# Kernel optimization log

Measured on AMD Instinct MI355X. Metric: run time of the kernel, lower is better.

## Reference

```python
import jax, jax.numpy as jnp
import numpy as np

TEMPERATURE = 0.07
N, D, NUM_CLASSES = 8192, 1024, 128


def setup_inputs() -> dict:
    key = jax.random.key(0)
    k1, k2 = jax.random.split(key)
    embeddings = jax.random.normal(k1, (N, D), dtype=jnp.float32)
    labels = jax.random.randint(k2, (N,), 0, NUM_CLASSES, dtype=jnp.int64)
    return {"embeddings": embeddings, "labels": labels}


def reference(embeddings, labels):
    # L2-normalize rows (eps matches F.normalize default clamp of 1e-12 on the norm)
    norm = jnp.maximum(jnp.linalg.norm(embeddings, axis=-1, keepdims=True), 1e-12)
    emb = embeddings / norm
    # [N, N] similarity scaled by temperature
    sim = jnp.matmul(emb, emb.T) / TEMPERATURE
    # positive mask: same label, diagonal zeroed
    pos_mask = (labels[:, None] == labels[None, :]).astype(sim.dtype)
    pos_mask = pos_mask * (1.0 - jnp.eye(sim.shape[0], dtype=sim.dtype))
    exp_sim = jnp.exp(sim)
    sum_exp = exp_sim.sum(axis=1)              # [N]
    pos_sum = (exp_sim * pos_mask).sum(axis=1)  # [N]
    loss = -jnp.log(pos_sum / sum_exp)
    return loss.mean()
```

## Files before the change

### kernel.cpp

```cpp
#include <hip/hip_runtime.h>
#include <hip/hip_bf16.h>
#include <math.h>

#define N 8192
#define D 1024
#define TILE 128
#define BK 32
#define NTILES (N / TILE)
#define NBLOCKS (NTILES * (NTILES + 1) / 2)

typedef __bf16 bf16_t;
typedef bf16_t bf16x4 __attribute__((ext_vector_type(4)));
typedef bf16_t bf16x8 __attribute__((ext_vector_type(8)));
typedef float f32x4 __attribute__((ext_vector_type(4)));

__global__ __launch_bounds__(256) void norm_cast(const float* __restrict__ in,
                                                 bf16_t* __restrict__ out) {
    const int row = blockIdx.x;
    const int tid = threadIdx.x;
    const float4 v = ((const float4*)(in + (size_t)row * D))[tid];
    float ss = v.x * v.x + v.y * v.y + v.z * v.z + v.w * v.w;
    #pragma unroll
    for (int off = 32; off >= 1; off >>= 1) ss += __shfl_xor(ss, off, 64);
    __shared__ float red[4];
    const int wave = tid >> 6, lane = tid & 63;
    if (lane == 0) red[wave] = ss;
    __syncthreads();
    const float tot = red[0] + red[1] + red[2] + red[3];
    const float scale = 1.0f / fmaxf(sqrtf(tot), 1e-12f);
    bf16x4 o;
    o[0] = (bf16_t)(v.x * scale);
    o[1] = (bf16_t)(v.y * scale);
    o[2] = (bf16_t)(v.z * scale);
    o[3] = (bf16_t)(v.w * scale);
    ((bf16x4*)(out + (size_t)row * D))[tid] = o;
}

__global__ __launch_bounds__(256) void gemm_fused(const bf16_t* __restrict__ E,
                                                  const int* __restrict__ labels,
                                                  float* __restrict__ sumExp,
                                                  float* __restrict__ posSum) {
    __shared__ bf16_t As[TILE * BK];
    __shared__ bf16_t Bs[TILE * BK];
    __shared__ int labR[TILE], labC[TILE];

    const int b = blockIdx.x;
    int ti = (int)((sqrtf(8.0f * (float)b + 1.0f) - 1.0f) * 0.5f);
    while ((ti + 1) * (ti + 2) / 2 <= b) ++ti;
    while (ti * (ti + 1) / 2 > b) --ti;
    const int tj = b - ti * (ti + 1) / 2;
    const bool isDiag = (ti == tj);

    const int tid     = threadIdx.x;
    const int wave    = tid >> 6;
    const int lane    = tid & 63;
    const int q       = lane >> 4;
    const int lr      = lane & 15;
    const int waveRow = wave >> 1;
    const int waveCol = wave & 1;
    const int rowStart = ti * TILE;
    const int colStart = tj * TILE;

    if (tid < TILE) labR[tid] = labels[rowStart + tid];
    else            labC[tid - TILE] = labels[colStart + (tid - TILE)];

    f32x4 acc[4][4];
    #pragma unroll
    for (int i = 0; i < 4; ++i)
        #pragma unroll
        for (int j = 0; j < 4; ++j)
            acc[i][j] = {0.f, 0.f, 0.f, 0.f};

    const char* baseA = (const char*)(E + (size_t)rowStart * D);
    const char* baseB = (const char*)(E + (size_t)colStart * D);

    const int runit = q ^ ((lr >> 1) & 3);

    for (int kk = 0; kk < D; kk += BK) {
        #pragma unroll
        for (int p = 0; p < 2; ++p) {
            const int u  = p * 256 + tid;
            const int r  = u >> 2;
            const int uc = (u & 3) ^ ((r >> 1) & 3);
            const char* ga = baseA + (size_t)r * (D * 2) + kk * 2 + uc * 16;
            const char* gb = baseB + (size_t)r * (D * 2) + kk * 2 + uc * 16;
            char* la = (char*)As + (p * 256 + wave * 64) * 16;
            char* lb = (char*)Bs + (p * 256 + wave * 64) * 16;
            __builtin_amdgcn_global_load_lds(
                (const __attribute__((address_space(1))) void*)ga,
                (__attribute__((address_space(3))) void*)la, 16, 0, 0);
            __builtin_amdgcn_global_load_lds(
                (const __attribute__((address_space(1))) void*)gb,
                (__attribute__((address_space(3))) void*)lb, 16, 0, 0);
        }
        __syncthreads();

        bf16x8 af[4], bfr[4];
        #pragma unroll
        for (int ri = 0; ri < 4; ++ri)
            af[ri] = *(const bf16x8*)((const char*)As +
                     (waveRow * 64 + ri * 16 + lr) * 64 + runit * 16);
        #pragma unroll
        for (int ci = 0; ci < 4; ++ci)
            bfr[ci] = *(const bf16x8*)((const char*)Bs +
                      (waveCol * 64 + ci * 16 + lr) * 64 + runit * 16);
        #pragma unroll
        for (int ri = 0; ri < 4; ++ri)
            #pragma unroll
            for (int ci = 0; ci < 4; ++ci)
                acc[ri][ci] = __builtin_amdgcn_mfma_f32_16x16x32_bf16(
                    af[ri], bfr[ci], acc[ri][ci], 0, 0, 0);
        __syncthreads();
    }

    const float invT = 1.0f / 0.07f;
    float colAll[4] = {0.f, 0.f, 0.f, 0.f};
    float colPos[4] = {0.f, 0.f, 0.f, 0.f};
    #pragma unroll
    for (int ri = 0; ri < 4; ++ri) {
        #pragma unroll
        for (int e = 0; e < 4; ++e) {
            const int rloc = waveRow * 64 + ri * 16 + q * 4 + e;
            const int gi   = rowStart + rloc;
            const int li   = labR[rloc];
            float s_all = 0.f, s_pos = 0.f;
            #pragma unroll
            for (int ci = 0; ci < 4; ++ci) {
                const int cloc = waveCol * 64 + ci * 16 + lr;
                const int gj   = colStart + cloc;
                const float v  = __expf(acc[ri][ci][e] * invT);
                const bool same = (labC[cloc] == li);
                s_all += v;
                if (same && gi != gj) s_pos += v;
                if (!isDiag) {
                    colAll[ci] += v;
                    if (same) colPos[ci] += v;
                }
            }
            #pragma unroll
            for (int off = 1; off < 16; off <<= 1) {
                s_all += __shfl_xor(s_all, off, 64);
                s_pos += __shfl_xor(s_pos, off, 64);
            }
            if (lr == 0) {
                atomicAdd(&sumExp[gi], s_all);
                atomicAdd(&posSum[gi], s_pos);
            }
        }
    }
    if (!isDiag) {
        #pragma unroll
        for (int ci = 0; ci < 4; ++ci) {
            float a = colAll[ci], p = colPos[ci];
            a += __shfl_xor(a, 16, 64);  a += __shfl_xor(a, 32, 64);
            p += __shfl_xor(p, 16, 64);  p += __shfl_xor(p, 32, 64);
            if (q == 0) {
                const int gj = colStart + waveCol * 64 + ci * 16 + lr;
                atomicAdd(&sumExp[gj], a);
                atomicAdd(&posSum[gj], p);
            }
        }
    }
}

__global__ __launch_bounds__(1024) void finalize(const float* __restrict__ sumExp,
                                                 const float* __restrict__ posSum,
                                                 float* __restrict__ out) {
    const int tid = threadIdx.x;
    float s = 0.f;
    #pragma unroll
    for (int i = tid; i < N; i += 1024)
        s += __logf(sumExp[i] / posSum[i]);
    #pragma unroll
    for (int off = 32; off >= 1; off >>= 1) s += __shfl_xor(s, off, 64);
    __shared__ float red[16];
    if ((tid & 63) == 0) red[tid >> 6] = s;
    __syncthreads();
    if (tid == 0) {
        float t = 0.f;
        #pragma unroll
        for (int i = 0; i < 16; ++i) t += red[i];
        out[0] = t / (float)N;
    }
}

extern "C" void kernel_launch(void* const* d_in, const int* in_sizes, int n_in,
                              void* d_out, int out_size, void* d_ws, size_t ws_size,
                              hipStream_t stream) {
    const float* emb    = (const float*)d_in[0];
    const int*   labels = (const int*)d_in[1];
    float* out = (float*)d_out;

    float*  sumExp = (float*)d_ws;
    float*  posSum = sumExp + N;
    bf16_t* EN     = (bf16_t*)((char*)d_ws + (size_t)2 * N * sizeof(float));

    hipMemsetAsync(d_ws, 0, (size_t)2 * N * sizeof(float), stream);

    norm_cast<<<N, 256, 0, stream>>>(emb, EN);

    gemm_fused<<<NBLOCKS, 256, 0, stream>>>(EN, labels, sumExp, posSum);

    finalize<<<1, 1024, 0, stream>>>(sumExp, posSum, out);
}
```

Measured before the change: 217.3 us.

## Load MFMA fragments directly from global memory, fold temperature into normalization, reorder tiles

Removes the LDS staging in the fused GEMM. Each wave now loads its bf16 MFMA fragments straight from global memory into registers with double buffering and no barriers in the K loop. The temperature and log2(e) factor are folded into the normalization scale (sqrt(log2e/T) per row), so the epilogue uses a raw exp2 instead of a multiply plus exp. Block-to-tile mapping is changed to group tiles in 8-wide column bands to improve L2 reuse, and a missing sync after the label loads is added. The cost is that rows are read redundantly from global/L2 by multiple waves with no LDS sharing, and pre-scaling before the bf16 cast changes rounding slightly.

```diff
diff --git a/kernel.cpp b/kernel.cpp
--- a/kernel.cpp
+++ b/kernel.cpp
@@ -5,7 +5,6 @@
 #define N 8192
 #define D 1024
 #define TILE 128
-#define BK 32
 #define NTILES (N / TILE)
 #define NBLOCKS (NTILES * (NTILES + 1) / 2)
 
@@ -13,6 +12,8 @@
 typedef bf16_t bf16x4 __attribute__((ext_vector_type(4)));
 typedef bf16_t bf16x8 __attribute__((ext_vector_type(8)));
 typedef float f32x4 __attribute__((ext_vector_type(4)));
+
+#define POST_SCALE 4.5398124f
 
 __global__ __launch_bounds__(256) void norm_cast(const float* __restrict__ in,
                                                  bf16_t* __restrict__ out) {
@@ -27,7 +28,7 @@
     if (lane == 0) red[wave] = ss;
     __syncthreads();
     const float tot = red[0] + red[1] + red[2] + red[3];
-    const float scale = 1.0f / fmaxf(sqrtf(tot), 1e-12f);
+    const float scale = POST_SCALE / fmaxf(sqrtf(tot), 1e-12f);
     bf16x4 o;
     o[0] = (bf16_t)(v.x * scale);
     o[1] = (bf16_t)(v.y * scale);
@@ -40,15 +41,24 @@
                                                   const int* __restrict__ labels,
                                                   float* __restrict__ sumExp,
                                                   float* __restrict__ posSum) {
-    __shared__ bf16_t As[TILE * BK];
-    __shared__ bf16_t Bs[TILE * BK];
     __shared__ int labR[TILE], labC[TILE];
 
     const int b = blockIdx.x;
-    int ti = (int)((sqrtf(8.0f * (float)b + 1.0f) - 1.0f) * 0.5f);
-    while ((ti + 1) * (ti + 2) / 2 <= b) ++ti;
-    while (ti * (ti + 1) / 2 > b) --ti;
-    const int tj = b - ti * (ti + 1) / 2;
+    int c = (int)((sqrtf(16.0f + 128.0f * (float)b) - 4.0f) * (1.0f / 64.0f));
+    while (32 * (c + 1) * (c + 1) + 4 * (c + 1) <= b) ++c;
+    while (32 * c * c + 4 * c > b) --c;
+    const int r = b - (32 * c * c + 4 * c);
+    int ti, tj;
+    if (r < 64 * c) {
+        tj = r >> 3;
+        ti = 8 * c + (r & 7);
+    } else {
+        int r2 = r - 64 * c;
+        int d = 0, off = 0;
+        while (off + (8 - d) <= r2) { off += 8 - d; ++d; }
+        tj = 8 * c + d;
+        ti = tj + (r2 - off);
+    }
     const bool isDiag = (ti == tj);
 
     const int tid     = threadIdx.x;
@@ -63,6 +73,7 @@
 
     if (tid < TILE) labR[tid] = labels[rowStart + tid];
     else            labC[tid - TILE] = labels[colStart + (tid - TILE)];
+    __syncthreads();
 
     f32x4 acc[4][4];
     #pragma unroll
@@ -71,49 +82,45 @@
         for (int j = 0; j < 4; ++j)
             acc[i][j] = {0.f, 0.f, 0.f, 0.f};
 
-    const char* baseA = (const char*)(E + (size_t)rowStart * D);
-    const char* baseB = (const char*)(E + (size_t)colStart * D);
-
-    const int runit = q ^ ((lr >> 1) & 3);
-
-    for (int kk = 0; kk < D; kk += BK) {
-        #pragma unroll
-        for (int p = 0; p < 2; ++p) {
-            const int u  = p * 256 + tid;
-            const int r  = u >> 2;
-            const int uc = (u & 3) ^ ((r >> 1) & 3);
-            const char* ga = baseA + (size_t)r * (D * 2) + kk * 2 + uc * 16;
-            const char* gb = baseB + (size_t)r * (D * 2) + kk * 2 + uc * 16;
-            char* la = (char*)As + (p * 256 + wave * 64) * 16;
-            char* lb = (char*)Bs + (p * 256 + wave * 64) * 16;
-            __builtin_amdgcn_global_load_lds(
-                (const __attribute__((address_space(1))) void*)ga,
-                (__attribute__((address_space(3))) void*)la, 16, 0, 0);
-            __builtin_amdgcn_global_load_lds(
-                (const __attribute__((address_space(1))) void*)gb,
-                (__attribute__((address_space(3))) void*)lb, 16, 0, 0);
+    const char* base = (const char*)E;
+    unsigned aOff[4], bOff[4];
+    #pragma unroll
+    for (int ri = 0; ri < 4; ++ri)
+        aOff[ri] = (unsigned)((rowStart + waveRow * 64 + ri * 16 + lr) * (D * 2)
+                              + q * 16);
+    #pragma unroll
+    for (int ci = 0; ci < 4; ++ci)
+        bOff[ci] = (unsigned)((colStart + waveCol * 64 + ci * 16 + lr) * (D * 2)
+                              + q * 16);
+
+    bf16x8 fa[2][4], fb[2][4];
+    #pragma unroll
+    for (int ri = 0; ri < 4; ++ri)
+        fa[0][ri] = *(const bf16x8*)(base + aOff[ri]);
+    #pragma unroll
+    for (int ci = 0; ci < 4; ++ci)
+        fb[0][ci] = *(const bf16x8*)(base + bOff[ci]);
+
+    #pragma unroll
+    for (int s = 0; s < 32; ++s) {
+        const int cur = s & 1, nxt = cur ^ 1;
+        if (s < 31) {
+            const unsigned kb = (unsigned)((s + 1) * 64);
+            #pragma unroll
+            for (int ri = 0; ri < 4; ++ri)
+                fa[nxt][ri] = *(const bf16x8*)(base + aOff[ri] + kb);
+            #pragma unroll
+            for (int ci = 0; ci < 4; ++ci)
+                fb[nxt][ci] = *(const bf16x8*)(base + bOff[ci] + kb);
         }
-        __syncthreads();
-
-        bf16x8 af[4], bfr[4];
-        #pragma unroll
-        for (int ri = 0; ri < 4; ++ri)
-            af[ri] = *(const bf16x8*)((const char*)As +
-                     (waveRow * 64 + ri * 16 + lr) * 64 + runit * 16);
-        #pragma unroll
-        for (int ci = 0; ci < 4; ++ci)
-            bfr[ci] = *(const bf16x8*)((const char*)Bs +
-                      (waveCol * 64 + ci * 16 + lr) * 64 + runit * 16);
         #pragma unroll
         for (int ri = 0; ri < 4; ++ri)
             #pragma unroll
             for (int ci = 0; ci < 4; ++ci)
                 acc[ri][ci] = __builtin_amdgcn_mfma_f32_16x16x32_bf16(
-                    af[ri], bfr[ci], acc[ri][ci], 0, 0, 0);
-        __syncthreads();
-    }
-
-    const float invT = 1.0f / 0.07f;
+                    fa[cur][ri], fb[cur][ci], acc[ri][ci], 0, 0, 0);
+    }
+
     float colAll[4] = {0.f, 0.f, 0.f, 0.f};
     float colPos[4] = {0.f, 0.f, 0.f, 0.f};
     #pragma unroll
@@ -128,13 +135,18 @@
             for (int ci = 0; ci < 4; ++ci) {
                 const int cloc = waveCol * 64 + ci * 16 + lr;
                 const int gj   = colStart + cloc;
-                const float v  = __expf(acc[ri][ci][e] * invT);
+#if __has_builtin(__builtin_amdgcn_exp2f)
+                const float v = __builtin_amdgcn_exp2f(acc[ri][ci][e]);
+#else
+                const float v = exp2f(acc[ri][ci][e]);
+#endif
                 const bool same = (labC[cloc] == li);
+                const float vp  = same ? v : 0.f;
                 s_all += v;
-                if (same && gi != gj) s_pos += v;
+                if (gi != gj) s_pos += vp;
                 if (!isDiag) {
                     colAll[ci] += v;
-                    if (same) colPos[ci] += v;
+                    colPos[ci] += vp;
                 }
             }
             #pragma unroll
```

New measurement: 398.0 us. 1.83x slower.

## Fold temperature into normalization, double K-tile, and fuse workspace zeroing

Applied to the files above, without the earlier changes.

Rows are scaled by sqrt(log2(e)/T) during normalization, so each dot product comes out in base-2 units and the epilogue can call a raw exp2 with no multiply. The K tile grows from 32 to 64 with a new XOR-swizzled LDS layout, which halves the number of barrier-synchronized iterations. The kernel also sets launch bounds for 4 blocks per CU, replaces branches with selects in the epilogue, and zeroes the sum buffers inside norm_cast instead of issuing a separate memset. The trade-offs are extra bf16 rounding error on the pre-scaled embeddings and more LDS per block, which could limit occupancy.

```diff
diff --git a/kernel.cpp b/kernel.cpp
--- a/kernel.cpp
+++ b/kernel.cpp
@@ -5,7 +5,7 @@
 #define N 8192
 #define D 1024
 #define TILE 128
-#define BK 32
+#define BK 64
 #define NTILES (N / TILE)
 #define NBLOCKS (NTILES * (NTILES + 1) / 2)
 
@@ -14,10 +14,14 @@
 typedef bf16_t bf16x8 __attribute__((ext_vector_type(8)));
 typedef float f32x4 __attribute__((ext_vector_type(4)));
 
+#define POST_SCALE 4.5398124f
+
 __global__ __launch_bounds__(256) void norm_cast(const float* __restrict__ in,
-                                                 bf16_t* __restrict__ out) {
+                                                 bf16_t* __restrict__ out,
+                                                 float* __restrict__ sums) {
     const int row = blockIdx.x;
     const int tid = threadIdx.x;
+    if (row < 64) sums[row * 256 + tid] = 0.f;
     const float4 v = ((const float4*)(in + (size_t)row * D))[tid];
     float ss = v.x * v.x + v.y * v.y + v.z * v.z + v.w * v.w;
     #pragma unroll
@@ -27,7 +31,7 @@
     if (lane == 0) red[wave] = ss;
     __syncthreads();
     const float tot = red[0] + red[1] + red[2] + red[3];
-    const float scale = 1.0f / fmaxf(sqrtf(tot), 1e-12f);
+    const float scale = POST_SCALE / fmaxf(sqrtf(tot), 1e-12f);
     bf16x4 o;
     o[0] = (bf16_t)(v.x * scale);
     o[1] = (bf16_t)(v.y * scale);
@@ -36,12 +40,10 @@
     ((bf16x4*)(out + (size_t)row * D))[tid] = o;
 }
 
-__global__ __launch_bounds__(256) void gemm_fused(const bf16_t* __restrict__ E,
-                                                  const int* __restrict__ labels,
-                                                  float* __restrict__ sumExp,
-                                                  float* __restrict__ posSum) {
-    __shared__ bf16_t As[TILE * BK];
-    __shared__ bf16_t Bs[TILE * BK];
+__global__ __launch_bounds__(256, 4) void gemm_fused(
+        const bf16_t* __restrict__ E, const int* __restrict__ labels,
+        float* __restrict__ sumExp, float* __restrict__ posSum) {
+    __shared__ char smem[2 * TILE * BK * 2];
     __shared__ int labR[TILE], labC[TILE];
 
     const int b = blockIdx.x;
@@ -71,21 +73,27 @@
         for (int j = 0; j < 4; ++j)
             acc[i][j] = {0.f, 0.f, 0.f, 0.f};
 
-    const char* baseA = (const char*)(E + (size_t)rowStart * D);
-    const char* baseB = (const char*)(E + (size_t)colStart * D);
-
-    const int runit = q ^ ((lr >> 1) & 3);
-
-    for (int kk = 0; kk < D; kk += BK) {
-        #pragma unroll
-        for (int p = 0; p < 2; ++p) {
-            const int u  = p * 256 + tid;
-            const int r  = u >> 2;
-            const int uc = (u & 3) ^ ((r >> 1) & 3);
-            const char* ga = baseA + (size_t)r * (D * 2) + kk * 2 + uc * 16;
-            const char* gb = baseB + (size_t)r * (D * 2) + kk * 2 + uc * 16;
-            char* la = (char*)As + (p * 256 + wave * 64) * 16;
-            char* lb = (char*)Bs + (p * 256 + wave * 64) * 16;
+    const int   srow = wave * 8 + (lane >> 3);
+    const int   uc   = (lane & 7) ^ (lane >> 3);
+    const char* gaBase = (const char*)(E + (size_t)rowStart * D) + srow * (D * 2) + uc * 16;
+    const char* gbBase = (const char*)(E + (size_t)colStart * D) + srow * (D * 2) + uc * 16;
+
+    unsigned aAddr[2], bAddr[2];
+    #pragma unroll
+    for (int h = 0; h < 2; ++h) {
+        const unsigned un = (unsigned)((h * 4 + q) ^ (lr & 7));
+        aAddr[h] = (unsigned)((waveRow * 64 + lr) * 128) + un * 16;
+        bAddr[h] = (unsigned)(16384 + (waveCol * 64 + lr) * 128) + un * 16;
+    }
+
+    for (int it = 0; it < 16; ++it) {
+        const unsigned kb = (unsigned)it * 128;
+        #pragma unroll
+        for (int p = 0; p < 4; ++p) {
+            const char* ga = gaBase + kb + p * (32 * D * 2);
+            const char* gb = gbBase + kb + p * (32 * D * 2);
+            char* la = smem + (p * 256 + wave * 64) * 16;
+            char* lb = smem + 16384 + (p * 256 + wave * 64) * 16;
             __builtin_amdgcn_global_load_lds(
                 (const __attribute__((address_space(1))) void*)ga,
                 (__attribute__((address_space(3))) void*)la, 16, 0, 0);
@@ -95,25 +103,25 @@
         }
         __syncthreads();
 
-        bf16x8 af[4], bfr[4];
-        #pragma unroll
-        for (int ri = 0; ri < 4; ++ri)
-            af[ri] = *(const bf16x8*)((const char*)As +
-                     (waveRow * 64 + ri * 16 + lr) * 64 + runit * 16);
-        #pragma unroll
-        for (int ci = 0; ci < 4; ++ci)
-            bfr[ci] = *(const bf16x8*)((const char*)Bs +
-                      (waveCol * 64 + ci * 16 + lr) * 64 + runit * 16);
-        #pragma unroll
-        for (int ri = 0; ri < 4; ++ri)
+        #pragma unroll
+        for (int h = 0; h < 2; ++h) {
+            bf16x8 af[4], bfr[4];
+            #pragma unroll
+            for (int ri = 0; ri < 4; ++ri)
+                af[ri] = *(const bf16x8*)(smem + aAddr[h] + ri * 2048);
             #pragma unroll
             for (int ci = 0; ci < 4; ++ci)
-                acc[ri][ci] = __builtin_amdgcn_mfma_f32_16x16x32_bf16(
-                    af[ri], bfr[ci], acc[ri][ci], 0, 0, 0);
+                bfr[ci] = *(const bf16x8*)(smem + bAddr[h] + ci * 2048);
+            #pragma unroll
+            for (int ri = 0; ri < 4; ++ri)
+                #pragma unroll
+                for (int ci = 0; ci < 4; ++ci)
+                    acc[ri][ci] = __builtin_amdgcn_mfma_f32_16x16x32_bf16(
+                        af[ri], bfr[ci], acc[ri][ci], 0, 0, 0);
+        }
         __syncthreads();
     }
 
-    const float invT = 1.0f / 0.07f;
     float colAll[4] = {0.f, 0.f, 0.f, 0.f};
     float colPos[4] = {0.f, 0.f, 0.f, 0.f};
     #pragma unroll
@@ -128,13 +136,18 @@
             for (int ci = 0; ci < 4; ++ci) {
                 const int cloc = waveCol * 64 + ci * 16 + lr;
                 const int gj   = colStart + cloc;
-                const float v  = __expf(acc[ri][ci][e] * invT);
+#if __has_builtin(__builtin_amdgcn_exp2f)
+                const float v = __builtin_amdgcn_exp2f(acc[ri][ci][e]);
+#else
+                const float v = exp2f(acc[ri][ci][e]);
+#endif
                 const bool same = (labC[cloc] == li);
+                const float vp  = same ? v : 0.f;
                 s_all += v;
-                if (same && gi != gj) s_pos += v;
+                if (gi != gj) s_pos += vp;
                 if (!isDiag) {
                     colAll[ci] += v;
-                    if (same) colPos[ci] += v;
+                    colPos[ci] += vp;
                 }
             }
             #pragma unroll
@@ -195,9 +208,7 @@
     float*  posSum = sumExp + N;
     bf16_t* EN     = (bf16_t*)((char*)d_ws + (size_t)2 * N * sizeof(float));
 
-    hipMemsetAsync(d_ws, 0, (size_t)2 * N * sizeof(float), stream);
-
-    norm_cast<<<N, 256, 0, stream>>>(emb, EN);
+    norm_cast<<<N, 256, 0, stream>>>(emb, EN, sumExp);
 
     gemm_fused<<<NBLOCKS, 256, 0, stream>>>(EN, labels, sumExp, posSum);
 
```

Result: slower. 228.1 us (+4.9%).
